# Kernel tuning notes

Measured on AMD Instinct MI355X. Metric: run time of the kernel, lower is better.

Reference implementation:

```python
import jax, jax.numpy as jnp
import numpy as np

N = 50000      # nodes
E = 800000     # edges (before self loops)
D = 128        # embedding_dimension
HEADS = 4
C = 32         # hidden_channels
NEG_SLOPE = 0.2


def setup_inputs() -> dict:
    key = jax.random.key(0)
    ks = jax.random.split(key, 12)
    s = 0.1
    x = jax.random.normal(ks[0], (N, D), jnp.float32)
    edge_index = jax.random.randint(ks[1], (2, E), 0, N)
    # layer 1: D -> HEADS*C, concat
    W1 = jax.random.normal(ks[2], (D, HEADS * C), jnp.float32) * s
    a_src1 = jax.random.normal(ks[3], (HEADS, C), jnp.float32) * s
    a_dst1 = jax.random.normal(ks[4], (HEADS, C), jnp.float32) * s
    b1 = jnp.zeros((HEADS * C,), jnp.float32)
    # layer 2: HEADS*C -> HEADS*C, concat
    W2 = jax.random.normal(ks[5], (HEADS * C, HEADS * C), jnp.float32) * s
    a_src2 = jax.random.normal(ks[6], (HEADS, C), jnp.float32) * s
    a_dst2 = jax.random.normal(ks[7], (HEADS, C), jnp.float32) * s
    b2 = jnp.zeros((HEADS * C,), jnp.float32)
    # layer 3: HEADS*C -> C, heads=1, no concat (mean over the single head)
    W3 = jax.random.normal(ks[8], (HEADS * C, C), jnp.float32) * s
    a_src3 = jax.random.normal(ks[9], (1, C), jnp.float32) * s
    a_dst3 = jax.random.normal(ks[10], (1, C), jnp.float32) * s
    b3 = jnp.zeros((C,), jnp.float32)
    return {"x": x, "edge_index": edge_index,
            "W1": W1, "a_src1": a_src1, "a_dst1": a_dst1, "b1": b1,
            "W2": W2, "a_src2": a_src2, "a_dst2": a_dst2, "b2": b2,
            "W3": W3, "a_src3": a_src3, "a_dst3": a_dst3, "b3": b3}


def gat_layer(x, src, dst, W, a_s, a_d, b, heads, concat):
    """One PyG-style GATConv (eval mode: dropout inactive).
    x: [N, Fin]; src/dst: [E2] (self loops included)."""
    n = x.shape[0]
    h = (x @ W).reshape(n, heads, -1)                 # [N, H, C]
    alpha_src = (h * a_s).sum(-1)                     # [N, H]
    alpha_dst = (h * a_d).sum(-1)                     # [N, H]
    logits = jax.nn.leaky_relu(alpha_src[src] + alpha_dst[dst], NEG_SLOPE)  # [E2, H]
    # segment softmax over destination nodes
    m = jax.ops.segment_max(logits, dst, num_segments=n)          # [N, H]
    ex = jnp.exp(logits - m[dst])                                  # [E2, H]
    denom = jax.ops.segment_sum(ex, dst, num_segments=n)          # [N, H]
    alpha = ex / (denom[dst] + 1e-16)                              # [E2, H]
    msg = h[src] * alpha[:, :, None]                               # [E2, H, C]
    out = jax.ops.segment_sum(msg, dst, num_segments=n)            # [N, H, C]
    if concat:
        return out.reshape(n, -1) + b
    return out.mean(axis=1) + b


def reference(x, edge_index, W1, a_src1, a_dst1, b1, W2, a_src2, a_dst2, b2,
              W3, a_src3, a_dst3, b3):
    loops = jnp.arange(N, dtype=edge_index.dtype)
    src = jnp.concatenate([edge_index[0], loops])   # add_self_loops=True
    dst = jnp.concatenate([edge_index[1], loops])
    h = gat_layer(x, src, dst, W1, a_src1, a_dst1, b1, HEADS, True)
    h = jax.nn.elu(h)
    h = gat_layer(h, src, dst, W2, a_src2, a_dst2, b2, HEADS, True)
    h = jax.nn.elu(h)
    out = gat_layer(h, src, dst, W3, a_src3, a_dst3, b3, 1, False)
    return out
```

## Files before the change

kernel.cpp:

```cpp
#include <hip/hip_runtime.h>
#include <cmath>

constexpr int NN  = 50000;
constexpr int EE  = 800000;
constexpr int E2C = EE + NN;
constexpr int DIM = 128;

constexpr int NBUCK = 256;
constexpr int BW    = 196;
constexpr int EPT   = 8;
constexpr int CH    = 256 * EPT;
constexpr int NB_B  = (E2C + CH - 1) / CH;
constexpr int CAP   = 4096;
constexpr int SCAP  = 5120;

using bf16x8 = __attribute__((ext_vector_type(8))) short;
using f32x4  = __attribute__((ext_vector_type(4))) float;

__device__ inline unsigned bf16rne(float f) {
    unsigned u = __builtin_bit_cast(unsigned, f);
    return (u + 0x7fffu + ((u >> 16) & 1u)) >> 16;
}
__device__ inline float bflo(unsigned u) { return __builtin_bit_cast(float, u << 16); }
__device__ inline float bfhi(unsigned u) { return __builtin_bit_cast(float, u & 0xffff0000u); }

__global__ __launch_bounds__(256) void cvt_weights(
    const float* __restrict__ W1, const float* __restrict__ W2,
    const float* __restrict__ W3,
    unsigned short* __restrict__ W1t, unsigned short* __restrict__ W2t,
    unsigned short* __restrict__ W3t, int* __restrict__ bcursor)
{
    int g = blockIdx.x * 256 + threadIdx.x;
    if (g < NBUCK) bcursor[g] = 0;
    const float* W; unsigned short* Wt; int cols;
    if (g < 2048)      { W = W1; Wt = W1t; cols = 128; }
    else if (g < 4096) { W = W2; Wt = W2t; cols = 128; g -= 2048; }
    else if (g < 4608) { W = W3; Wt = W3t; cols = 32;  g -= 4096; }
    else return;
    int c  = g / 16;
    int k8 = (g % 16) * 8;
    unsigned up[4];
    #pragma unroll
    for (int j = 0; j < 4; ++j) {
        float a = W[(k8 + 2 * j) * cols + c];
        float b = W[(k8 + 2 * j + 1) * cols + c];
        up[j] = bf16rne(a) | (bf16rne(b) << 16);
    }
    uint4 u; u.x = up[0]; u.y = up[1]; u.z = up[2]; u.w = up[3];
    *(uint4*)(Wt + c * 128 + k8) = u;
}

template<int NT, int NH, bool F32IN>
__global__ __launch_bounds__(256) void gemm_mfma(
    const void* __restrict__ inv, const unsigned short* __restrict__ Wt,
    const float* __restrict__ a_s, const float* __restrict__ a_d,
    unsigned short* __restrict__ hout, float* __restrict__ asrc,
    float* __restrict__ adst)
{
    constexpr int COLS = NT * 16;
    constexpr int TPH  = NT / NH;
    const int lane = threadIdx.x & 63;
    const int wave = threadIdx.x >> 6;
    const int m    = lane & 15;
    const int quad = lane >> 4;
    const int n0   = blockIdx.x * 64 + wave * 16;

    int arow = n0 + m; if (arow >= NN) arow = NN - 1;

    f32x4 acc[NT] = {};
    #pragma unroll
    for (int kq = 0; kq < 4; ++kq) {
        bf16x8 a;
        if constexpr (F32IN) {
            const float* ap = (const float*)inv + (long long)arow * 128 + quad * 8 + kq * 32;
            float4 v0 = *(const float4*)ap;
            float4 v1 = *(const float4*)(ap + 4);
            a[0] = (short)bf16rne(v0.x); a[1] = (short)bf16rne(v0.y);
            a[2] = (short)bf16rne(v0.z); a[3] = (short)bf16rne(v0.w);
            a[4] = (short)bf16rne(v1.x); a[5] = (short)bf16rne(v1.y);
            a[6] = (short)bf16rne(v1.z); a[7] = (short)bf16rne(v1.w);
        } else {
            a = *(const bf16x8*)((const unsigned short*)inv
                    + (long long)arow * 128 + quad * 8 + kq * 32);
        }
        #pragma unroll
        for (int t = 0; t < NT; ++t) {
            bf16x8 b = *(const bf16x8*)(Wt + (t * 16 + m) * 128 + kq * 32 + quad * 8);
            acc[t] = __builtin_amdgcn_mfma_f32_16x16x32_bf16(a, b, acc[t], 0, 0, 0);
        }
    }

    #pragma unroll
    for (int r = 0; r < 4; ++r) {
        int node = n0 + quad * 4 + r;
        if (node < NN) {
            #pragma unroll
            for (int t = 0; t < NT; ++t)
                hout[(long long)node * COLS + t * 16 + m] =
                    (unsigned short)bf16rne(acc[t][r]);
        }
    }

    float asv[NT], adv[NT];
    #pragma unroll
    for (int t = 0; t < NT; ++t) { asv[t] = a_s[t * 16 + m]; adv[t] = a_d[t * 16 + m]; }

    #pragma unroll
    for (int r = 0; r < 4; ++r) {
        const int node = n0 + quad * 4 + r;
        #pragma unroll
        for (int hh = 0; hh < NH; ++hh) {
            float ps = 0.f, pd = 0.f;
            #pragma unroll
            for (int q = 0; q < TPH; ++q) {
                int t = hh * TPH + q;
                ps = fmaf(acc[t][r], asv[t], ps);
                pd = fmaf(acc[t][r], adv[t], pd);
            }
            #pragma unroll
            for (int off = 8; off > 0; off >>= 1) {
                ps += __shfl_down(ps, off, 16);
                pd += __shfl_down(pd, off, 16);
            }
            if (m == 0 && node < NN) {
                asrc[node * NH + hh] = ps;
                adst[node * NH + hh] = pd;
            }
        }
    }

    if (blockIdx.x == 0 && threadIdx.x == 0) {
        #pragma unroll
        for (int hh = 0; hh < NH; ++hh) asrc[NN * NH + hh] = -1e30f;
    }
}

__global__ __launch_bounds__(256) void bucket_bin(
    const int* __restrict__ ei, int* __restrict__ bcursor,
    unsigned* __restrict__ pairs)
{
    __shared__ int cnt[NBUCK];
    __shared__ int scanex[NBUCK];
    __shared__ int base[NBUCK];
    __shared__ int cur[NBUCK];
    __shared__ unsigned stage[CH];

    const int tid = threadIdx.x;
    const long long e0 = (long long)blockIdx.x * CH;
    cnt[tid] = 0;
    __syncthreads();

    unsigned rec[EPT]; int bk[EPT];
    #pragma unroll
    for (int j = 0; j < EPT; ++j) {
        long long e = e0 + tid + j * 256;
        bool valid = e < E2C;
        int ss = 0, dd = 0;
        if (valid) {
            if (e < EE) { ss = ei[e]; dd = ei[EE + e]; }
            else        { ss = dd = (int)(e - EE); }
        }
        int b = dd / BW;
        bk[j]  = valid ? b : -1;
        rec[j] = (unsigned)ss | ((unsigned)(dd - b * BW) << 16) | ((unsigned)b << 24);
        if (valid) atomicAdd(&cnt[b], 1);
    }
    __syncthreads();

    const int myc = cnt[tid];
    scanex[tid] = myc;
    __syncthreads();
    for (int off = 1; off < NBUCK; off <<= 1) {
        int t = (tid >= off) ? scanex[tid - off] : 0;
        __syncthreads();
        scanex[tid] += t;
        __syncthreads();
    }
    int excl = scanex[tid] - myc;
    __syncthreads();
    scanex[tid] = excl;
    cur[tid]    = excl;
    base[tid]   = atomicAdd(&bcursor[tid], myc);
    __syncthreads();

    #pragma unroll
    for (int j = 0; j < EPT; ++j) {
        if (bk[j] >= 0) {
            int p = atomicAdd(&cur[bk[j]], 1);
            stage[p] = rec[j];
        }
    }
    __syncthreads();

    const int total = (e0 + CH <= E2C) ? CH : (int)(E2C - e0);
    for (int j = tid; j < total; j += 256) {
        unsigned p = stage[j];
        int b = (int)(p >> 24);
        pairs[(size_t)b * CAP + base[b] + (j - scanex[b])] = p;
    }
}

__global__ __launch_bounds__(256) void bucket_sort(
    const int* __restrict__ bcursor, const unsigned* __restrict__ pairs,
    int2* __restrict__ rowp, unsigned short* __restrict__ sorted_src,
    unsigned short* __restrict__ perm)
{
    __shared__ int deg[256];
    __shared__ int scn[256];
    __shared__ int cur[256];
    __shared__ int hist2[64];
    __shared__ int scn2[64];
    __shared__ int cur2[64];
    const int b  = blockIdx.x;
    const int n0 = b * BW;
    const int n1 = (n0 + BW < NN) ? n0 + BW : NN;
    const int nloc = n1 - n0;
    const int tid = threadIdx.x;
    const int mycnt = bcursor[b];
    const unsigned* seg = pairs + (size_t)b * CAP;
    const int base = b * SCAP;

    deg[tid] = 0;
    if (tid < 64) hist2[tid] = 0;
    __syncthreads();
    for (int i = tid; i < mycnt; i += 256)
        atomicAdd(&deg[(seg[i] >> 16) & 0xff], 1);
    __syncthreads();

    const int pv = (deg[tid] + 3) & ~3;
    int it = pv >> 2; if (it > 63) it = 63;
    scn[tid] = pv;
    if (tid < nloc) atomicAdd(&hist2[it], 1);
    __syncthreads();
    for (int off = 1; off < 256; off <<= 1) {
        int t = (tid >= off) ? scn[tid - off] : 0;
        __syncthreads();
        scn[tid] += t;
        __syncthreads();
    }
    if (tid < 64) scn2[tid] = hist2[tid];
    __syncthreads();
    for (int off = 1; off < 64; off <<= 1) {
        int t = (tid >= off && tid < 64) ? scn2[tid - off] : 0;
        __syncthreads();
        if (tid < 64) scn2[tid] += t;
        __syncthreads();
    }
    if (tid < 64) cur2[tid] = scn2[tid] - hist2[tid];
    __syncthreads();

    const int totalp = scn[255];
    const int pexcl  = scn[tid] - pv;
    cur[tid] = base + pexcl;
    if (tid < nloc) {
        int rank = atomicAdd(&cur2[it], 1);
        perm[n0 + rank] = (unsigned short)(n0 + tid);
        rowp[n0 + rank] = make_int2(base + pexcl, base + pexcl + pv);
    }
    __syncthreads();

    for (int i = tid; i < totalp; i += 256)
        sorted_src[base + i] = (unsigned short)NN;
    __syncthreads();
    for (int i = tid; i < mycnt; i += 256) {
        unsigned p = seg[i];
        int pos = atomicAdd(&cur[(p >> 16) & 0xff], 1);
        sorted_src[pos] = (unsigned short)(p & 0xffff);
    }
}

template<int COLS, int NH, bool DO_ELU, bool OUTBF>
__global__ __launch_bounds__(256) void aggr_csr(
    const unsigned short* __restrict__ perm,
    const int2* __restrict__ rowp, const unsigned short* __restrict__ sorted_src,
    const unsigned short* __restrict__ hin,
    const float* __restrict__ asrc, const float* __restrict__ adst,
    const float* __restrict__ bias, void* __restrict__ outv)
{
    constexpr int TPN = COLS / 16;
    constexpr int USTR = COLS / 2;
    int t = blockIdx.x * 256 + threadIdx.x;
    int rk = t / TPN;
    int lc = t % TPN;
    if (rk >= NN) return;
    const int d = perm[rk];
    const int cc = lc * 16;
    const int head = cc / 32;
    const float ad = adst[d * NH + head];
    const int2 be = rowp[rk];
    const int beg = be.x, end = be.y;
    const uint* hp = (const uint*)hin + cc / 2;

    float num[16] = {};
    float den = 0.f;

    ushort4 sv = *(const ushort4*)&sorted_src[beg];
    for (int i = beg; i < end; i += 4) {
        ushort4 nx = *(const ushort4*)&sorted_src[i + 4];
        const int s[4] = {sv.x, sv.y, sv.z, sv.w};
        float a[4];
        uint4 Hv[4][2];
        #pragma unroll
        for (int j = 0; j < 4; ++j) a[j] = asrc[s[j] * NH + head];
        #pragma unroll
        for (int j = 0; j < 4; ++j) {
            const uint* row = hp + (long long)s[j] * USTR;
            Hv[j][0] = *(const uint4*)row;
            Hv[j][1] = *(const uint4*)(row + 4);
        }
        #pragma unroll
        for (int j = 0; j < 4; ++j) {
            float l = a[j] + ad; l = l > 0.f ? l : 0.2f * l;
            float w = __builtin_expf(l);
            den += w;
            #pragma unroll
            for (int q = 0; q < 2; ++q) {
                num[q*8+0] = fmaf(w, bflo(Hv[j][q].x), num[q*8+0]);
                num[q*8+1] = fmaf(w, bfhi(Hv[j][q].x), num[q*8+1]);
                num[q*8+2] = fmaf(w, bflo(Hv[j][q].y), num[q*8+2]);
                num[q*8+3] = fmaf(w, bfhi(Hv[j][q].y), num[q*8+3]);
                num[q*8+4] = fmaf(w, bflo(Hv[j][q].z), num[q*8+4]);
                num[q*8+5] = fmaf(w, bfhi(Hv[j][q].z), num[q*8+5]);
                num[q*8+6] = fmaf(w, bflo(Hv[j][q].w), num[q*8+6]);
                num[q*8+7] = fmaf(w, bfhi(Hv[j][q].w), num[q*8+7]);
            }
        }
        sv = nx;
    }

    float inv = 1.f / (den + 1e-16f);
    float v[16];
    #pragma unroll
    for (int j = 0; j < 16; ++j) {
        v[j] = num[j] * inv + bias[cc + j];
        if (DO_ELU) v[j] = v[j] > 0.f ? v[j] : expm1f(v[j]);
    }
    if constexpr (OUTBF) {
        uint4 u0, u1;
        u0.x = bf16rne(v[0])  | (bf16rne(v[1])  << 16);
        u0.y = bf16rne(v[2])  | (bf16rne(v[3])  << 16);
        u0.z = bf16rne(v[4])  | (bf16rne(v[5])  << 16);
        u0.w = bf16rne(v[6])  | (bf16rne(v[7])  << 16);
        u1.x = bf16rne(v[8])  | (bf16rne(v[9])  << 16);
        u1.y = bf16rne(v[10]) | (bf16rne(v[11]) << 16);
        u1.z = bf16rne(v[12]) | (bf16rne(v[13]) << 16);
        u1.w = bf16rne(v[14]) | (bf16rne(v[15]) << 16);
        unsigned short* op = (unsigned short*)outv + (long long)d * COLS + cc;
        *(uint4*)op       = u0;
        *(uint4*)(op + 8) = u1;
    } else {
        float* out = (float*)outv + (long long)d * COLS + cc;
        *(float4*)(out + 0)  = make_float4(v[0],  v[1],  v[2],  v[3]);
        *(float4*)(out + 4)  = make_float4(v[4],  v[5],  v[6],  v[7]);
        *(float4*)(out + 8)  = make_float4(v[8],  v[9],  v[10], v[11]);
        *(float4*)(out + 12) = make_float4(v[12], v[13], v[14], v[15]);
    }
}

extern "C" void kernel_launch(void* const* d_in, const int* in_sizes, int n_in,
                              void* d_out, int out_size, void* d_ws, size_t ws_size,
                              hipStream_t stream)
{
    const float* x   = (const float*)d_in[0];
    const int*   ei  = (const int*)  d_in[1];
    const float* W1  = (const float*)d_in[2];
    const float* as1 = (const float*)d_in[3];
    const float* ad1 = (const float*)d_in[4];
    const float* b1  = (const float*)d_in[5];
    const float* W2  = (const float*)d_in[6];
    const float* as2 = (const float*)d_in[7];
    const float* ad2 = (const float*)d_in[8];
    const float* b2  = (const float*)d_in[9];
    const float* W3  = (const float*)d_in[10];
    const float* as3 = (const float*)d_in[11];
    const float* ad3 = (const float*)d_in[12];
    const float* b3  = (const float*)d_in[13];
    float* out = (float*)d_out;

    unsigned short* H16 = (unsigned short*)d_ws;
    unsigned short* O16 = H16 + (size_t)(NN + 1) * 128;
    unsigned short* P16 = O16 + (size_t)NN * 128;
    unsigned short* W1t = P16 + (size_t)NN * 128;
    unsigned short* W2t = W1t + 128 * 128;
    unsigned short* W3t = W2t + 128 * 128;
    float* ASRC = (float*)(W3t + 32 * 128);
    float* ADST = ASRC + (size_t)(NN + 1) * 4;
    int2* rowp  = (int2*)(ADST + (size_t)NN * 4);
    unsigned short* sorted = (unsigned short*)(rowp + NN);
    int* bcursor = (int*)(sorted + (size_t)NBUCK * SCAP + 8);
    unsigned short* perm = (unsigned short*)(bcursor + NBUCK);
    size_t off = ((size_t)(perm + NN) - (size_t)d_ws + 15) & ~(size_t)15;
    unsigned* pairs = (unsigned*)((char*)d_ws + off);

    const int gCvtW    = (4608 + 255) / 256;
    const int gGemm    = (NN + 63) / 64;
    const int gAggr128 = (NN * 8 + 255) / 256;
    const int gAggr32  = (NN * 2 + 255) / 256;

    cvt_weights<<<gCvtW, 256, 0, stream>>>(W1, W2, W3, W1t, W2t, W3t, bcursor);
    bucket_bin<<<NB_B, 256, 0, stream>>>(ei, bcursor, pairs);
    bucket_sort<<<NBUCK, 256, 0, stream>>>(bcursor, pairs, rowp, sorted, perm);

    gemm_mfma<8, 4, true><<<gGemm, 256, 0, stream>>>(x, W1t, as1, ad1, H16, ASRC, ADST);
    aggr_csr<128, 4, true, true><<<gAggr128, 256, 0, stream>>>(
        perm, rowp, sorted, H16, ASRC, ADST, b1, O16);

    gemm_mfma<8, 4, false><<<gGemm, 256, 0, stream>>>(O16, W2t, as2, ad2, H16, ASRC, ADST);
    aggr_csr<128, 4, true, true><<<gAggr128, 256, 0, stream>>>(
        perm, rowp, sorted, H16, ASRC, ADST, b2, P16);

    gemm_mfma<2, 1, false><<<gGemm, 256, 0, stream>>>(P16, W3t, as3, ad3, H16, ASRC, ADST);
    aggr_csr<32, 1, false, false><<<gAggr32, 256, 0, stream>>>(
        perm, rowp, sorted, H16, ASRC, ADST, b3, out);
}
```

Measured before the change: 286.9 us.

## Halve columns per thread and software-pipeline neighbor gathers in CSR aggregation

New measurement: 279.6 us. 1.03x faster.

```diff
diff --git a/kernel.cpp b/kernel.cpp
--- a/kernel.cpp
+++ b/kernel.cpp
@@ -259,8 +259,11 @@
     }
     __syncthreads();
 
-    for (int i = tid; i < totalp; i += 256)
+    int lim = totalp + 8; if (lim > SCAP) lim = SCAP;
+    for (int i = tid; i < lim; i += 256)
         sorted_src[base + i] = (unsigned short)NN;
+    if (b == NBUCK - 1 && tid < 8)
+        sorted_src[NBUCK * SCAP + tid] = (unsigned short)NN;
     __syncthreads();
     for (int i = tid; i < mycnt; i += 256) {
         unsigned p = seg[i];
@@ -277,83 +280,75 @@
     const float* __restrict__ asrc, const float* __restrict__ adst,
     const float* __restrict__ bias, void* __restrict__ outv)
 {
-    constexpr int TPN = COLS / 16;
+    constexpr int TPN = COLS / 8;
     constexpr int USTR = COLS / 2;
     int t = blockIdx.x * 256 + threadIdx.x;
     int rk = t / TPN;
     int lc = t % TPN;
     if (rk >= NN) return;
     const int d = perm[rk];
-    const int cc = lc * 16;
+    const int cc = lc * 8;
     const int head = cc / 32;
     const float ad = adst[d * NH + head];
     const int2 be = rowp[rk];
     const int beg = be.x, end = be.y;
     const uint* hp = (const uint*)hin + cc / 2;
 
-    float num[16] = {};
+    float num[8] = {};
     float den = 0.f;
 
-    ushort4 sv = *(const ushort4*)&sorted_src[beg];
+    ushort4 v0 = *(const ushort4*)&sorted_src[beg];
+    int s0[4] = {v0.x, v0.y, v0.z, v0.w};
+    float a0[4]; uint4 H0[4];
+    #pragma unroll
+    for (int j = 0; j < 4; ++j) a0[j] = asrc[s0[j] * NH + head];
+    #pragma unroll
+    for (int j = 0; j < 4; ++j) H0[j] = *(const uint4*)&hp[(long long)s0[j] * USTR];
+    ushort4 sv = *(const ushort4*)&sorted_src[beg + 4];
+
     for (int i = beg; i < end; i += 4) {
-        ushort4 nx = *(const ushort4*)&sorted_src[i + 4];
-        const int s[4] = {sv.x, sv.y, sv.z, sv.w};
-        float a[4];
-        uint4 Hv[4][2];
-        #pragma unroll
-        for (int j = 0; j < 4; ++j) a[j] = asrc[s[j] * NH + head];
+        ushort4 nxt = *(const ushort4*)&sorted_src[i + 8];
+        int s1[4] = {sv.x, sv.y, sv.z, sv.w};
+        float a1[4]; uint4 H1[4];
+        #pragma unroll
+        for (int j = 0; j < 4; ++j) a1[j] = asrc[s1[j] * NH + head];
+        #pragma unroll
+        for (int j = 0; j < 4; ++j) H1[j] = *(const uint4*)&hp[(long long)s1[j] * USTR];
         #pragma unroll
         for (int j = 0; j < 4; ++j) {
-            const uint* row = hp + (long long)s[j] * USTR;
-            Hv[j][0] = *(const uint4*)row;
-            Hv[j][1] = *(const uint4*)(row + 4);
-        }
-        #pragma unroll
-        for (int j = 0; j < 4; ++j) {
-            float l = a[j] + ad; l = l > 0.f ? l : 0.2f * l;
+            float l = a0[j] + ad; l = l > 0.f ? l : 0.2f * l;
             float w = __builtin_expf(l);
             den += w;
-            #pragma unroll
-            for (int q = 0; q < 2; ++q) {
-                num[q*8+0] = fmaf(w, bflo(Hv[j][q].x), num[q*8+0]);
-                num[q*8+1] = fmaf(w, bfhi(Hv[j][q].x), num[q*8+1]);
-                num[q*8+2] = fmaf(w, bflo(Hv[j][q].y), num[q*8+2]);
-                num[q*8+3] = fmaf(w, bfhi(Hv[j][q].y), num[q*8+3]);
-                num[q*8+4] = fmaf(w, bflo(Hv[j][q].z), num[q*8+4]);
-                num[q*8+5] = fmaf(w, bfhi(Hv[j][q].z), num[q*8+5]);
-                num[q*8+6] = fmaf(w, bflo(Hv[j][q].w), num[q*8+6]);
-                num[q*8+7] = fmaf(w, bfhi(Hv[j][q].w), num[q*8+7]);
-            }
-        }
-        sv = nx;
+            num[0] = fmaf(w, bflo(H0[j].x), num[0]); num[1] = fmaf(w, bfhi(H0[j].x), num[1]);
+            num[2] = fmaf(w, bflo(H0[j].y), num[2]); num[3] = fmaf(w, bfhi(H0[j].y), num[3]);
+            num[4] = fmaf(w, bflo(H0[j].z), num[4]); num[5] = fmaf(w, bfhi(H0[j].z), num[5]);
+            num[6] = fmaf(w, bflo(H0[j].w), num[6]); num[7] = fmaf(w, bfhi(H0[j].w), num[7]);
+        }
+        #pragma unroll
+        for (int j = 0; j < 4; ++j) { s0[j] = s1[j]; a0[j] = a1[j]; H0[j] = H1[j]; }
+        sv = nxt;
     }
 
     float inv = 1.f / (den + 1e-16f);
-    float v[16];
-    #pragma unroll
-    for (int j = 0; j < 16; ++j) {
+    float v[8];
+    #pragma unroll
+    for (int j = 0; j < 8; ++j) {
         v[j] = num[j] * inv + bias[cc + j];
         if (DO_ELU) v[j] = v[j] > 0.f ? v[j] : expm1f(v[j]);
     }
     if constexpr (OUTBF) {
-        uint4 u0, u1;
-        u0.x = bf16rne(v[0])  | (bf16rne(v[1])  << 16);
-        u0.y = bf16rne(v[2])  | (bf16rne(v[3])  << 16);
-        u0.z = bf16rne(v[4])  | (bf16rne(v[5])  << 16);
-        u0.w = bf16rne(v[6])  | (bf16rne(v[7])  << 16);
-        u1.x = bf16rne(v[8])  | (bf16rne(v[9])  << 16);
-        u1.y = bf16rne(v[10]) | (bf16rne(v[11]) << 16);
-        u1.z = bf16rne(v[12]) | (bf16rne(v[13]) << 16);
-        u1.w = bf16rne(v[14]) | (bf16rne(v[15]) << 16);
-        unsigned short* op = (unsigned short*)outv + (long long)d * COLS + cc;
-        *(uint4*)op       = u0;
-        *(uint4*)(op + 8) = u1;
+        uint4 u;
+        u.x = bf16rne(v[0]) | (bf16rne(v[1]) << 16);
+        u.y = bf16rne(v[2]) | (bf16rne(v[3]) << 16);
+        u.z = bf16rne(v[4]) | (bf16rne(v[5]) << 16);
+        u.w = bf16rne(v[6]) | (bf16rne(v[7]) << 16);
+        *(uint4*)((unsigned short*)outv + (long long)d * COLS + cc) = u;
     } else {
-        float* out = (float*)outv + (long long)d * COLS + cc;
-        *(float4*)(out + 0)  = make_float4(v[0],  v[1],  v[2],  v[3]);
-        *(float4*)(out + 4)  = make_float4(v[4],  v[5],  v[6],  v[7]);
-        *(float4*)(out + 8)  = make_float4(v[8],  v[9],  v[10], v[11]);
-        *(float4*)(out + 12) = make_float4(v[12], v[13], v[14], v[15]);
+        float4 o0 = {v[0], v[1], v[2], v[3]};
+        float4 o1 = {v[4], v[5], v[6], v[7]};
+        float* out = (float*)outv;
+        *(float4*)&out[(long long)d * COLS + cc]     = o0;
+        *(float4*)&out[(long long)d * COLS + cc + 4] = o1;
     }
 }
 
@@ -394,8 +389,8 @@
 
     const int gCvtW    = (4608 + 255) / 256;
     const int gGemm    = (NN + 63) / 64;
-    const int gAggr128 = (NN * 8 + 255) / 256;
-    const int gAggr32  = (NN * 2 + 255) / 256;
+    const int gAggr128 = (NN * 16 + 255) / 256;
+    const int gAggr32  = (NN * 4 + 255) / 256;
 
     cvt_weights<<<gCvtW, 256, 0, stream>>>(W1, W2, W3, W1t, W2t, W3t, bcursor);
     bucket_bin<<<NB_B, 256, 0, stream>>>(ei, bcursor, pairs);
```
